# Kernel optimization log

Hardware: AMD Instinct MI355X
Metric: run time of the kernel (lower is better)

Reference implementation:

```python
import jax, jax.numpy as jnp
import numpy as np

D_MODEL = 512
D_FF = 2048
VOCAB = 32000
B, N = 2, 384
EPS = 1e-6


def positional_encoding(n, d):
    pos = np.arange(n)[:, None].astype(np.float64)
    i = np.arange(d)[None, :]
    ang = pos / np.power(10000.0, (2 * (i // 2)) / np.float32(d))
    ang[:, 0::2] = np.sin(ang[:, 0::2])
    ang[:, 1::2] = np.cos(ang[:, 1::2])
    return jnp.asarray(ang, dtype=jnp.float32)  # [n, d]


def layer_norm(x, gamma, beta):
    mu = jnp.mean(x, axis=-1, keepdims=True)
    var = jnp.mean(jnp.square(x - mu), axis=-1, keepdims=True)
    return (x - mu) / jnp.sqrt(var + EPS) * gamma + beta


def setup_inputs() -> dict:
    key = jax.random.key(0)
    ks = jax.random.split(key, 12)
    s = 0.02
    return {
        "tokens": jax.random.randint(ks[0], (B, N), 0, VOCAB, dtype=jnp.int32),
        "emb": jax.random.normal(ks[1], (VOCAB, D_MODEL), jnp.float32) * s,
        "Wq": jax.random.normal(ks[2], (D_MODEL, D_MODEL), jnp.float32) * s,
        "bq": jnp.zeros((D_MODEL,), jnp.float32),
        "Wk": jax.random.normal(ks[3], (D_MODEL, D_MODEL), jnp.float32) * s,
        "bk": jnp.zeros((D_MODEL,), jnp.float32),
        "Wv": jax.random.normal(ks[4], (D_MODEL, D_MODEL), jnp.float32) * s,
        "bv": jnp.zeros((D_MODEL,), jnp.float32),
        "attn_scale": jax.random.normal(ks[5], (D_MODEL,), jnp.float32) * 0.05,
        "Wo": jax.random.normal(ks[6], (D_MODEL, D_MODEL), jnp.float32) * s,
        "bo": jnp.zeros((D_MODEL,), jnp.float32),
        "g1": jnp.ones((D_MODEL,), jnp.float32),
        "beta1": jnp.zeros((D_MODEL,), jnp.float32),
        "W1": jax.random.normal(ks[7], (D_MODEL, D_FF), jnp.float32) * s,
        "bf1": jnp.zeros((D_FF,), jnp.float32),
        "W2": jax.random.normal(ks[8], (D_FF, D_MODEL), jnp.float32) * s,
        "bf2": jnp.zeros((D_MODEL,), jnp.float32),
        "g2": jnp.ones((D_MODEL,), jnp.float32),
        "beta2": jnp.zeros((D_MODEL,), jnp.float32),
    }


def reference(tokens, emb, Wq, bq, Wk, bk, Wv, bv, attn_scale, Wo, bo,
              g1, beta1, W1, bf1, W2, bf2, g2, beta2):
    # Embedding + scaled positional encoding
    x = emb[tokens] * jnp.sqrt(jnp.float32(D_MODEL))  # [B, N, D]
    x = x + positional_encoding(N, D_MODEL)[None, :, :]

    # Additive (Bahdanau) self-attention
    q = x @ Wq + bq
    k = x @ Wk + bk  # note: original swaps key/value Dense layers; math-equivalent
    v = x @ Wv + bv
    # scores[b,i,j] = sum_d scale[d] * tanh(q[b,i,d] + k[b,j,d])  -> [B,N,N]
    scores = jnp.einsum("d,bijd->bij", attn_scale,
                        jnp.tanh(q[:, :, None, :] + k[:, None, :, :]))
    weights = jax.nn.softmax(scores, axis=-1)
    attn = jnp.einsum("bij,bjd->bid", weights, v)
    attn = attn @ Wo + bo
    x = layer_norm(x + attn, g1, beta1)

    # Feedforward + residual + LayerNorm
    h = jax.nn.relu(x @ W1 + bf1)
    y = h @ W2 + bf2
    return layer_norm(x + y, g2, beta2)
```

## Files before the change

### kernel.cpp

```cpp
#include <hip/hip_runtime.h>
#include <hip/hip_bf16.h>
#include <math.h>

#define D_MODEL 512
#define D_FF    2048
#define NBATCH  2
#define NSEQ    384
#define NROWS   (NBATCH * NSEQ)
#define LN_EPS  1e-6f

typedef __attribute__((ext_vector_type(8))) short short8;
typedef __attribute__((ext_vector_type(4))) short short4v;
typedef __attribute__((ext_vector_type(4))) float f32x4;
typedef __hip_bfloat16 bf16;

static __device__ __forceinline__ short bfb(float x) {
    bf16 h = __float2bfloat16(x);
    return *reinterpret_cast<short*>(&h);
}

__global__ __launch_bounds__(256) void prep_kernel(
    const int* __restrict__ tokens, const float* __restrict__ emb,
    const float* __restrict__ Wq, const float* __restrict__ Wk,
    const float* __restrict__ Wv, const float* __restrict__ Wo,
    const float* __restrict__ W1, const float* __restrict__ W2,
    bf16* __restrict__ wqt, bf16* __restrict__ wkt, bf16* __restrict__ wvt,
    bf16* __restrict__ wot, bf16* __restrict__ w1t, bf16* __restrict__ w2t,
    float* __restrict__ x, bf16* __restrict__ xb)
{
    __shared__ float tile[32][33];
    int t = blockIdx.x;

    if (t < 3072) {
        const float* W; bf16* Wt; int K, N, bx, by;
        if (t < 1024) {
            int w = t >> 8, rem = t & 255;
            W  = (w == 0) ? Wq  : (w == 1) ? Wk  : (w == 2) ? Wv  : Wo;
            Wt = (w == 0) ? wqt : (w == 1) ? wkt : (w == 2) ? wvt : wot;
            K = 512; N = 512; bx = rem & 15; by = rem >> 4;
        } else if (t < 2048) {
            int rem = t - 1024;
            W = W1; Wt = w1t; K = 512; N = 2048; bx = rem & 63; by = rem >> 6;
        } else {
            int rem = t - 2048;
            W = W2; Wt = w2t; K = 2048; N = 512; bx = rem & 15; by = rem >> 4;
        }
        int tx = threadIdx.x & 31, ty = threadIdx.x >> 5;
        #pragma unroll
        for (int r = ty; r < 32; r += 8)
            tile[r][tx] = W[(size_t)(by * 32 + r) * N + bx * 32 + tx];
        __syncthreads();
        #pragma unroll
        for (int r = ty; r < 32; r += 8)
            Wt[(size_t)(bx * 32 + r) * K + by * 32 + tx] = __float2bfloat16(tile[tx][r]);
    } else {
        int row = t - 3072;
        int n   = row % NSEQ;
        int tok = tokens[row];
        const float sqrtD = 22.627416997969522f;
        const float ESC   = 0.02595256324130752f;
        for (int d = threadIdx.x; d < D_MODEL; d += 256) {
            float e   = emb[tok * D_MODEL + d] * sqrtD;
            float ang = (float)n * __builtin_amdgcn_exp2f(-(float)(d & ~1) * ESC);
            float pe  = (d & 1) ? __cosf(ang) : __sinf(ang);
            float val = e + pe;
            x [(size_t)row * D_MODEL + d] = val;
            xb[(size_t)row * D_MODEL + d] = __float2bfloat16(val);
        }
    }
}

__global__ __launch_bounds__(256) void qkv_mfma_kernel(
    const bf16* __restrict__ A,
    const bf16* __restrict__ wqt, const bf16* __restrict__ wkt, const bf16* __restrict__ wvt,
    const float* __restrict__ bq, const float* __restrict__ bk, const float* __restrict__ bv,
    float* __restrict__ aexp, float* __restrict__ bexp, bf16* __restrict__ vT)
{
    int z = blockIdx.z;
    const bf16*  Wt   = (z == 0) ? wqt : (z == 1) ? wkt : wvt;
    const float* bias = (z == 0) ? bq  : (z == 1) ? bk  : bv;

    int lane = threadIdx.x & 63, wid = threadIdx.x >> 6;
    int rowBase = blockIdx.y * 32 + (wid >> 1) * 16;
    int colBase = blockIdx.x * 64 + (wid & 1) * 32;

    const bf16* Ap  = A  + (size_t)(rowBase + (lane & 15)) * D_MODEL + ((lane >> 4) << 3);
    const bf16* Bp0 = Wt + (size_t)(colBase + (lane & 15)) * D_MODEL + ((lane >> 4) << 3);
    const bf16* Bp1 = Bp0 + (size_t)16 * D_MODEL;

    f32x4 acc0 = {0.f, 0.f, 0.f, 0.f};
    f32x4 acc1 = {0.f, 0.f, 0.f, 0.f};

    #pragma unroll 4
    for (int k0 = 0; k0 < D_MODEL; k0 += 32) {
        short8 a  = *reinterpret_cast<const short8*>(Ap  + k0);
        short8 b0 = *reinterpret_cast<const short8*>(Bp0 + k0);
        short8 b1 = *reinterpret_cast<const short8*>(Bp1 + k0);
        acc0 = __builtin_amdgcn_mfma_f32_16x16x32_bf16(a, b0, acc0, 0, 0, 0);
        acc1 = __builtin_amdgcn_mfma_f32_16x16x32_bf16(a, b1, acc1, 0, 0, 0);
    }

    int crow = rowBase + ((lane >> 4) << 2);
    int ccol = colBase + (lane & 15);

    if (z < 2) {
        float* C = (z == 0) ? aexp : bexp;
        #pragma unroll
        for (int r = 0; r < 4; ++r) {
            int row = crow + r;
            #pragma unroll
            for (int j = 0; j < 2; ++j) {
                int col = ccol + j * 16;
                float val = (j == 0 ? acc0[r] : acc1[r]) + bias[col];
                C[(size_t)row * D_MODEL + col] = __expf(2.0f * val);
            }
        }
    } else {
        int bb = crow / NSEQ;
        int jr = crow - bb * NSEQ;
        #pragma unroll
        for (int j = 0; j < 2; ++j) {
            int col = ccol + j * 16;
            short4v pk;
            #pragma unroll
            for (int r = 0; r < 4; ++r)
                pk[r] = bfb((j == 0 ? acc0[r] : acc1[r]) + bias[col]);
            size_t idx = ((size_t)bb * D_MODEL + col) * NSEQ + jr;
            *reinterpret_cast<short4v*>((short*)vT + idx) = pk;
        }
    }
}

__global__ __launch_bounds__(512) void score_kernel(
    const float* __restrict__ aexp, const float* __restrict__ bexp,
    const float* __restrict__ scale, bf16* __restrict__ E,
    float* __restrict__ Sp)
{
    int ig   = blockIdx.x;
    int qt   = blockIdx.y;
    int row0 = ig * 4;
    int b    = row0 / NSEQ;
    int tid  = threadIdx.x;
    int lane = tid & 63, wid = tid >> 6;

    __shared__ float sred[8][4];

    const float* ap = aexp + (size_t)row0 * D_MODEL + lane * 8;
    float a[4][8];
    #pragma unroll
    for (int r = 0; r < 4; ++r) {
        float4 A0 = *(const float4*)(ap + (size_t)r * D_MODEL);
        float4 A1 = *(const float4*)(ap + (size_t)r * D_MODEL + 4);
        a[r][0]=A0.x; a[r][1]=A0.y; a[r][2]=A0.z; a[r][3]=A0.w;
        a[r][4]=A1.x; a[r][5]=A1.y; a[r][6]=A1.z; a[r][7]=A1.w;
    }
    float4 S0 = *(const float4*)(scale + lane * 8);
    float4 S1 = *(const float4*)(scale + lane * 8 + 4);
    float sv[8] = {-2.0f*S0.x,-2.0f*S0.y,-2.0f*S0.z,-2.0f*S0.w,
                   -2.0f*S1.x,-2.0f*S1.y,-2.0f*S1.z,-2.0f*S1.w};

    const float* kb = bexp + (size_t)b * NSEQ * D_MODEL + lane * 8;
    int jb = qt * 96 + wid;

    float es[4] = {0.f, 0.f, 0.f, 0.f};

    for (int t6 = 0; t6 < 6; ++t6) {
        int j0 = jb + t6 * 16;
        int j1 = j0 + 8;
        const float4* kp0 = (const float4*)(kb + (size_t)j0 * D_MODEL);
        const float4* kp1 = (const float4*)(kb + (size_t)j1 * D_MODEL);
        float4 xa = kp0[0], xc = kp0[1];
        float4 ya = kp1[0], yc = kp1[1];
        float b0[8] = {xa.x,xa.y,xa.z,xa.w,xc.x,xc.y,xc.z,xc.w};
        float b1[8] = {ya.x,ya.y,ya.z,ya.w,yc.x,yc.y,yc.z,yc.w};

        float u[4][2] = {};
        #pragma unroll
        for (int up = 0; up < 4; ++up) {
            int d0 = up * 2, d1 = d0 + 1;
            #pragma unroll
            for (int js = 0; js < 2; ++js) {
                float xx = js ? b1[d0] : b0[d0];
                float yy = js ? b1[d1] : b0[d1];
                #pragma unroll
                for (int r = 0; r < 4; ++r) {
                    float p   = fmaf(a[r][d0], xx, 1.0f);
                    float q   = fmaf(a[r][d1], yy, 1.0f);
                    float num = fmaf(sv[d0], q, sv[d1] * p);
                    u[r][js]  = fmaf(num, __builtin_amdgcn_rcpf(p * q), u[r][js]);
                }
            }
        }

        #pragma unroll
        for (int off = 1; off < 64; off <<= 1) {
            #pragma unroll
            for (int r = 0; r < 4; ++r) {
                u[r][0] += __shfl_xor(u[r][0], off, 64);
                u[r][1] += __shfl_xor(u[r][1], off, 64);
            }
        }

        #pragma unroll
        for (int r = 0; r < 4; ++r) {
            float e0 = __expf(u[r][0]);
            float e1 = __expf(u[r][1]);
            if (lane == 0) {
                E[(size_t)(row0 + r) * NSEQ + j0] = __float2bfloat16(e0);
                E[(size_t)(row0 + r) * NSEQ + j1] = __float2bfloat16(e1);
            }
            es[r] += e0 + e1;
        }
    }

    if (lane == 0) {
        sred[wid][0] = es[0]; sred[wid][1] = es[1];
        sred[wid][2] = es[2]; sred[wid][3] = es[3];
    }
    __syncthreads();
    if (tid < 4) {
        float s = 0.0f;
        #pragma unroll
        for (int w = 0; w < 8; ++w) s += sred[w][tid];
        Sp[(size_t)(row0 + tid) * 4 + qt] = s;
    }
}

__global__ __launch_bounds__(256) void pv_mfma_kernel(
    const bf16* __restrict__ E, const bf16* __restrict__ vT,
    const float* __restrict__ Sp, bf16* __restrict__ attnb)
{
    int z = blockIdx.z;
    int lane = threadIdx.x & 63, wid = threadIdx.x >> 6;
    int rowBase = blockIdx.y * 32 + (wid >> 1) * 16;
    int colBase = blockIdx.x * 64 + (wid & 1) * 32;

    const bf16* Ap  = E  + ((size_t)z * NSEQ + rowBase + (lane & 15)) * NSEQ + ((lane >> 4) << 3);
    const bf16* Bp0 = vT + ((size_t)z * D_MODEL + colBase + (lane & 15)) * NSEQ + ((lane >> 4) << 3);
    const bf16* Bp1 = Bp0 + (size_t)16 * NSEQ;

    f32x4 acc0 = {0.f, 0.f, 0.f, 0.f};
    f32x4 acc1 = {0.f, 0.f, 0.f, 0.f};

    #pragma unroll 4
    for (int k0 = 0; k0 < NSEQ; k0 += 32) {
        short8 a  = *reinterpret_cast<const short8*>(Ap  + k0);
        short8 b0 = *reinterpret_cast<const short8*>(Bp0 + k0);
        short8 b1 = *reinterpret_cast<const short8*>(Bp1 + k0);
        acc0 = __builtin_amdgcn_mfma_f32_16x16x32_bf16(a, b0, acc0, 0, 0, 0);
        acc1 = __builtin_amdgcn_mfma_f32_16x16x32_bf16(a, b1, acc1, 0, 0, 0);
    }

    int crow = rowBase + ((lane >> 4) << 2);
    int ccol = colBase + (lane & 15);
    #pragma unroll
    for (int r = 0; r < 4; ++r) {
        int grow = z * NSEQ + crow + r;
        float4 sp4 = *(const float4*)(Sp + (size_t)grow * 4);
        float Sinv = 1.0f / (sp4.x + sp4.y + sp4.z + sp4.w);
        #pragma unroll
        for (int j = 0; j < 2; ++j)
            attnb[(size_t)grow * D_MODEL + ccol + j * 16] =
                __float2bfloat16((j == 0 ? acc0[r] : acc1[r]) * Sinv);
    }
}

__global__ __launch_bounds__(256) void mfma_gemm_kernel(
    const bf16* __restrict__ A, const bf16* __restrict__ Wt,
    const float* __restrict__ bias, const float* __restrict__ resid,
    float* __restrict__ Cf, bf16* __restrict__ Cb,
    int K, int N, int relu)
{
    int lane = threadIdx.x & 63, wid = threadIdx.x >> 6;
    int rowBase = blockIdx.y * 32 + (wid >> 1) * 16;
    int colBase = blockIdx.x * 64 + (wid & 1) * 32;

    const bf16* Ap  = A  + (size_t)(rowBase + (lane & 15)) * K + ((lane >> 4) << 3);
    const bf16* Bp0 = Wt + (size_t)(colBase + (lane & 15)) * K + ((lane >> 4) << 3);
    const bf16* Bp1 = Bp0 + (size_t)16 * K;

    f32x4 acc0 = {0.f, 0.f, 0.f, 0.f};
    f32x4 acc1 = {0.f, 0.f, 0.f, 0.f};

    #pragma unroll 4
    for (int k0 = 0; k0 < K; k0 += 32) {
        short8 a  = *reinterpret_cast<const short8*>(Ap  + k0);
        short8 b0 = *reinterpret_cast<const short8*>(Bp0 + k0);
        short8 b1 = *reinterpret_cast<const short8*>(Bp1 + k0);
        acc0 = __builtin_amdgcn_mfma_f32_16x16x32_bf16(a, b0, acc0, 0, 0, 0);
        acc1 = __builtin_amdgcn_mfma_f32_16x16x32_bf16(a, b1, acc1, 0, 0, 0);
    }

    int crow = rowBase + ((lane >> 4) << 2);
    int ccol = colBase + (lane & 15);
    #pragma unroll
    for (int r = 0; r < 4; ++r) {
        int row = crow + r;
        #pragma unroll
        for (int j = 0; j < 2; ++j) {
            int col = ccol + j * 16;
            float val = (j == 0 ? acc0[r] : acc1[r]) + bias[col];
            if (resid) val += resid[(size_t)row * N + col];
            if (relu)  val = fmaxf(val, 0.0f);
            if (Cf) Cf[(size_t)row * N + col] = val;
            if (Cb) Cb[(size_t)row * N + col] = __float2bfloat16(val);
        }
    }
}

__global__ __launch_bounds__(256) void ln_kernel(
    const float* __restrict__ in, const float* __restrict__ gamma,
    const float* __restrict__ beta, float* __restrict__ out,
    bf16* __restrict__ outb)
{
    int row = blockIdx.x;
    int tid = threadIdx.x;
    int lane = tid & 63, wid = tid >> 6;
    __shared__ float red[4];

    float v0 = in[(size_t)row * D_MODEL + tid];
    float v1 = in[(size_t)row * D_MODEL + tid + 256];

    float s = v0 + v1;
    #pragma unroll
    for (int off = 32; off; off >>= 1) s += __shfl_xor(s, off, 64);
    if (lane == 0) red[wid] = s;
    __syncthreads();
    if (tid == 0) red[0] = red[0] + red[1] + red[2] + red[3];
    __syncthreads();
    float mu = red[0] * (1.0f / D_MODEL);
    __syncthreads();

    float d0 = v0 - mu, d1 = v1 - mu;
    float s2 = d0 * d0 + d1 * d1;
    #pragma unroll
    for (int off = 32; off; off >>= 1) s2 += __shfl_xor(s2, off, 64);
    if (lane == 0) red[wid] = s2;
    __syncthreads();
    if (tid == 0) red[0] = red[0] + red[1] + red[2] + red[3];
    __syncthreads();
    float var = red[0] * (1.0f / D_MODEL);
    float inv = rsqrtf(var + LN_EPS);

    float o0 = d0 * inv * gamma[tid] + beta[tid];
    float o1 = d1 * inv * gamma[tid + 256] + beta[tid + 256];
    out[(size_t)row * D_MODEL + tid]       = o0;
    out[(size_t)row * D_MODEL + tid + 256] = o1;
    if (outb) {
        outb[(size_t)row * D_MODEL + tid]       = __float2bfloat16(o0);
        outb[(size_t)row * D_MODEL + tid + 256] = __float2bfloat16(o1);
    }
}

extern "C" void kernel_launch(void* const* d_in, const int* in_sizes, int n_in,
                              void* d_out, int out_size, void* d_ws, size_t ws_size,
                              hipStream_t stream)
{
    const int*   tokens = (const int*)  d_in[0];
    const float* emb    = (const float*)d_in[1];
    const float* Wq     = (const float*)d_in[2];
    const float* bq     = (const float*)d_in[3];
    const float* Wk     = (const float*)d_in[4];
    const float* bk     = (const float*)d_in[5];
    const float* Wv     = (const float*)d_in[6];
    const float* bv     = (const float*)d_in[7];
    const float* ascale = (const float*)d_in[8];
    const float* Wo     = (const float*)d_in[9];
    const float* bo     = (const float*)d_in[10];
    const float* g1     = (const float*)d_in[11];
    const float* beta1  = (const float*)d_in[12];
    const float* W1     = (const float*)d_in[13];
    const float* bf1    = (const float*)d_in[14];
    const float* W2     = (const float*)d_in[15];
    const float* bf2    = (const float*)d_in[16];
    const float* g2     = (const float*)d_in[17];
    const float* beta2  = (const float*)d_in[18];

    float* out = (float*)d_out;
    float* ws  = (float*)d_ws;

    const size_t SZ = (size_t)NROWS * D_MODEL;

    float* x0   = ws;
    float* aexp = ws + 1 * SZ;
    float* bexp = ws + 2 * SZ;
    float* t1 = aexp;
    float* x1 = bexp;
    float* y  = x0;

    bf16* x0b   = (bf16*)(ws + 3 * SZ);
    bf16* attnb = x0b + SZ;
    bf16* x1b   = attnb + SZ;
    bf16* hb    = x1b + SZ;
    bf16* Eb    = hb + (size_t)NROWS * D_FF;
    bf16* vTb   = Eb + (size_t)NBATCH * NSEQ * NSEQ;
    bf16* wqt   = vTb + (size_t)NBATCH * D_MODEL * NSEQ;
    bf16* wkt   = wqt + (size_t)D_MODEL * D_MODEL;
    bf16* wvt   = wkt + (size_t)D_MODEL * D_MODEL;
    bf16* wot   = wvt + (size_t)D_MODEL * D_MODEL;
    bf16* w1t   = wot + (size_t)D_MODEL * D_MODEL;
    bf16* w2t   = w1t + (size_t)D_MODEL * D_FF;
    float* Sp   = (float*)(w2t + (size_t)D_FF * D_MODEL);

    prep_kernel<<<3072 + NROWS, 256, 0, stream>>>(
        tokens, emb, Wq, Wk, Wv, Wo, W1, W2,
        wqt, wkt, wvt, wot, w1t, w2t, x0, x0b);

    qkv_mfma_kernel<<<dim3(D_MODEL / 64, NROWS / 32, 3), 256, 0, stream>>>(
        x0b, wqt, wkt, wvt, bq, bk, bv, aexp, bexp, vTb);

    score_kernel<<<dim3(NROWS / 4, 4), 512, 0, stream>>>(aexp, bexp, ascale, Eb, Sp);

    pv_mfma_kernel<<<dim3(D_MODEL / 64, NSEQ / 32, NBATCH), 256, 0, stream>>>(
        Eb, vTb, Sp, attnb);

    mfma_gemm_kernel<<<dim3(D_MODEL / 64, NROWS / 32), 256, 0, stream>>>(
        attnb, wot, bo, x0, t1, nullptr, D_MODEL, D_MODEL, 0);

    ln_kernel<<<NROWS, 256, 0, stream>>>(t1, g1, beta1, x1, x1b);

    mfma_gemm_kernel<<<dim3(D_FF / 64, NROWS / 32), 256, 0, stream>>>(
        x1b, w1t, bf1, nullptr, nullptr, hb, D_MODEL, D_FF, 1);

    mfma_gemm_kernel<<<dim3(D_MODEL / 64, NROWS / 32), 256, 0, stream>>>(
        hb, w2t, bf2, x1, y, nullptr, D_FF, D_MODEL, 0);

    ln_kernel<<<NROWS, 256, 0, stream>>>(y, g2, beta2, out, nullptr);
}
```

Before: 125.8 us.

## Fuse PV, Wo projection and first LayerNorm; split-K the FF down GEMM

Attention-weighted V, the Wo projection with bias and residual, and the first LayerNorm now run in one kernel. Each 512-thread block handles 16 rows and keeps the intermediate attention output and pre-norm activations in shared memory. This removes two launches and the global round trips for attnb and t1, at the cost of only 48 blocks, which may leave much of the GPU idle. The FF down-projection is split into two K halves to double the block count, and the partial sums are added inside the final LayerNorm kernel.

```diff
diff --git a/kernel.cpp b/kernel.cpp
--- a/kernel.cpp
+++ b/kernel.cpp
@@ -18,6 +18,8 @@
     bf16 h = __float2bfloat16(x);
     return *reinterpret_cast<short*>(&h);
 }
+
+#define MFMA16(a, b, c) __builtin_amdgcn_mfma_f32_16x16x32_bf16((a), (b), (c), 0, 0, 0)
 
 __global__ __launch_bounds__(256) void prep_kernel(
     const int* __restrict__ tokens, const float* __restrict__ emb,
@@ -96,8 +98,8 @@
         short8 a  = *reinterpret_cast<const short8*>(Ap  + k0);
         short8 b0 = *reinterpret_cast<const short8*>(Bp0 + k0);
         short8 b1 = *reinterpret_cast<const short8*>(Bp1 + k0);
-        acc0 = __builtin_amdgcn_mfma_f32_16x16x32_bf16(a, b0, acc0, 0, 0, 0);
-        acc1 = __builtin_amdgcn_mfma_f32_16x16x32_bf16(a, b1, acc1, 0, 0, 0);
+        acc0 = MFMA16(a, b0, acc0);
+        acc1 = MFMA16(a, b1, acc1);
     }
 
     int crow = rowBase + ((lane >> 4) << 2);
@@ -226,50 +228,117 @@
     }
 }
 
-__global__ __launch_bounds__(256) void pv_mfma_kernel(
+__global__ __launch_bounds__(512) void pv_wo_ln_kernel(
     const bf16* __restrict__ E, const bf16* __restrict__ vT,
-    const float* __restrict__ Sp, bf16* __restrict__ attnb)
-{
-    int z = blockIdx.z;
-    int lane = threadIdx.x & 63, wid = threadIdx.x >> 6;
-    int rowBase = blockIdx.y * 32 + (wid >> 1) * 16;
-    int colBase = blockIdx.x * 64 + (wid & 1) * 32;
-
-    const bf16* Ap  = E  + ((size_t)z * NSEQ + rowBase + (lane & 15)) * NSEQ + ((lane >> 4) << 3);
-    const bf16* Bp0 = vT + ((size_t)z * D_MODEL + colBase + (lane & 15)) * NSEQ + ((lane >> 4) << 3);
-    const bf16* Bp1 = Bp0 + (size_t)16 * NSEQ;
-
-    f32x4 acc0 = {0.f, 0.f, 0.f, 0.f};
-    f32x4 acc1 = {0.f, 0.f, 0.f, 0.f};
-
-    #pragma unroll 4
-    for (int k0 = 0; k0 < NSEQ; k0 += 32) {
-        short8 a  = *reinterpret_cast<const short8*>(Ap  + k0);
-        short8 b0 = *reinterpret_cast<const short8*>(Bp0 + k0);
-        short8 b1 = *reinterpret_cast<const short8*>(Bp1 + k0);
-        acc0 = __builtin_amdgcn_mfma_f32_16x16x32_bf16(a, b0, acc0, 0, 0, 0);
-        acc1 = __builtin_amdgcn_mfma_f32_16x16x32_bf16(a, b1, acc1, 0, 0, 0);
-    }
-
-    int crow = rowBase + ((lane >> 4) << 2);
-    int ccol = colBase + (lane & 15);
+    const float* __restrict__ Sp, const bf16* __restrict__ wot,
+    const float* __restrict__ bo, const float* __restrict__ x0,
+    const float* __restrict__ g1, const float* __restrict__ beta1,
+    float* __restrict__ x1, bf16* __restrict__ x1b)
+{
+    int row0 = blockIdx.x * 16;
+    int b    = row0 / NSEQ;
+    int tid  = threadIdx.x;
+    int lane = tid & 63, wid = tid >> 6;
+    int colBase = wid * 64;
+
+    __shared__ bf16  attnS[16][D_MODEL + 8];
+    __shared__ float t1f  [16][D_MODEL + 4];
+
+    int arow = lane & 15;
+    int koff = (lane >> 4) << 3;
+    int crow = (lane >> 4) << 2;
+    int ccol = lane & 15;
+
+    {
+        const bf16* Ap = E + ((size_t)(row0 + arow)) * NSEQ + koff;
+        const bf16* Bp = vT + ((size_t)b * D_MODEL + colBase + arow) * NSEQ + koff;
+        f32x4 p0 = {0,0,0,0}, p1 = {0,0,0,0}, p2 = {0,0,0,0}, p3 = {0,0,0,0};
+        #pragma unroll
+        for (int k0 = 0; k0 < NSEQ; k0 += 32) {
+            short8 a  = *(const short8*)(Ap + k0);
+            short8 v0 = *(const short8*)(Bp + k0);
+            short8 v1 = *(const short8*)(Bp + (size_t)16 * NSEQ + k0);
+            short8 v2 = *(const short8*)(Bp + (size_t)32 * NSEQ + k0);
+            short8 v3 = *(const short8*)(Bp + (size_t)48 * NSEQ + k0);
+            p0 = MFMA16(a, v0, p0);
+            p1 = MFMA16(a, v1, p1);
+            p2 = MFMA16(a, v2, p2);
+            p3 = MFMA16(a, v3, p3);
+        }
+        #pragma unroll
+        for (int r = 0; r < 4; ++r) {
+            int lrow = crow + r;
+            float4 sp4 = *(const float4*)(Sp + (size_t)(row0 + lrow) * 4);
+            float Sinv = 1.0f / (sp4.x + sp4.y + sp4.z + sp4.w);
+            attnS[lrow][colBase +  0 + ccol] = __float2bfloat16(p0[r] * Sinv);
+            attnS[lrow][colBase + 16 + ccol] = __float2bfloat16(p1[r] * Sinv);
+            attnS[lrow][colBase + 32 + ccol] = __float2bfloat16(p2[r] * Sinv);
+            attnS[lrow][colBase + 48 + ccol] = __float2bfloat16(p3[r] * Sinv);
+        }
+    }
+    __syncthreads();
+
+    {
+        const bf16* Wp = wot + ((size_t)(colBase + arow)) * D_MODEL + koff;
+        f32x4 w0 = {0,0,0,0}, w1 = {0,0,0,0}, w2 = {0,0,0,0}, w3 = {0,0,0,0};
+        #pragma unroll
+        for (int k0 = 0; k0 < D_MODEL; k0 += 32) {
+            short8 a  = *(const short8*)(&attnS[arow][k0 + koff]);
+            short8 q0 = *(const short8*)(Wp + k0);
+            short8 q1 = *(const short8*)(Wp + (size_t)16 * D_MODEL + k0);
+            short8 q2 = *(const short8*)(Wp + (size_t)32 * D_MODEL + k0);
+            short8 q3 = *(const short8*)(Wp + (size_t)48 * D_MODEL + k0);
+            w0 = MFMA16(a, q0, w0);
+            w1 = MFMA16(a, q1, w1);
+            w2 = MFMA16(a, q2, w2);
+            w3 = MFMA16(a, q3, w3);
+        }
+        #pragma unroll
+        for (int r = 0; r < 4; ++r) {
+            int lrow = crow + r;
+            size_t grow = (size_t)(row0 + lrow);
+            int c0 = colBase + ccol;
+            t1f[lrow][c0     ] = w0[r] + bo[c0     ] + x0[grow * D_MODEL + c0     ];
+            t1f[lrow][c0 + 16] = w1[r] + bo[c0 + 16] + x0[grow * D_MODEL + c0 + 16];
+            t1f[lrow][c0 + 32] = w2[r] + bo[c0 + 32] + x0[grow * D_MODEL + c0 + 32];
+            t1f[lrow][c0 + 48] = w3[r] + bo[c0 + 48] + x0[grow * D_MODEL + c0 + 48];
+        }
+    }
+    __syncthreads();
+
     #pragma unroll
-    for (int r = 0; r < 4; ++r) {
-        int grow = z * NSEQ + crow + r;
-        float4 sp4 = *(const float4*)(Sp + (size_t)grow * 4);
-        float Sinv = 1.0f / (sp4.x + sp4.y + sp4.z + sp4.w);
-        #pragma unroll
-        for (int j = 0; j < 2; ++j)
-            attnb[(size_t)grow * D_MODEL + ccol + j * 16] =
-                __float2bfloat16((j == 0 ? acc0[r] : acc1[r]) * Sinv);
+    for (int rr = 0; rr < 2; ++rr) {
+        int lrow = wid * 2 + rr;
+        size_t grow = (size_t)(row0 + lrow);
+        float v[8];
+        #pragma unroll
+        for (int u = 0; u < 8; ++u) v[u] = t1f[lrow][lane * 8 + u];
+        float s = 0.0f;
+        #pragma unroll
+        for (int u = 0; u < 8; ++u) s += v[u];
+        #pragma unroll
+        for (int off = 1; off < 64; off <<= 1) s += __shfl_xor(s, off, 64);
+        float mu = s * (1.0f / D_MODEL);
+        float s2 = 0.0f;
+        #pragma unroll
+        for (int u = 0; u < 8; ++u) { float d = v[u] - mu; s2 += d * d; }
+        #pragma unroll
+        for (int off = 1; off < 64; off <<= 1) s2 += __shfl_xor(s2, off, 64);
+        float inv = rsqrtf(s2 * (1.0f / D_MODEL) + LN_EPS);
+        #pragma unroll
+        for (int u = 0; u < 8; ++u) {
+            int c = lane * 8 + u;
+            float o = (v[u] - mu) * inv * g1[c] + beta1[c];
+            x1 [grow * D_MODEL + c] = o;
+            x1b[grow * D_MODEL + c] = __float2bfloat16(o);
+        }
     }
 }
 
 __global__ __launch_bounds__(256) void mfma_gemm_kernel(
     const bf16* __restrict__ A, const bf16* __restrict__ Wt,
-    const float* __restrict__ bias, const float* __restrict__ resid,
-    float* __restrict__ Cf, bf16* __restrict__ Cb,
-    int K, int N, int relu)
+    const float* __restrict__ bias,
+    bf16* __restrict__ Cb, int K, int N, int relu)
 {
     int lane = threadIdx.x & 63, wid = threadIdx.x >> 6;
     int rowBase = blockIdx.y * 32 + (wid >> 1) * 16;
@@ -287,8 +356,8 @@
         short8 a  = *reinterpret_cast<const short8*>(Ap  + k0);
         short8 b0 = *reinterpret_cast<const short8*>(Bp0 + k0);
         short8 b1 = *reinterpret_cast<const short8*>(Bp1 + k0);
-        acc0 = __builtin_amdgcn_mfma_f32_16x16x32_bf16(a, b0, acc0, 0, 0, 0);
-        acc1 = __builtin_amdgcn_mfma_f32_16x16x32_bf16(a, b1, acc1, 0, 0, 0);
+        acc0 = MFMA16(a, b0, acc0);
+        acc1 = MFMA16(a, b1, acc1);
     }
 
     int crow = rowBase + ((lane >> 4) << 2);
@@ -300,18 +369,62 @@
         for (int j = 0; j < 2; ++j) {
             int col = ccol + j * 16;
             float val = (j == 0 ? acc0[r] : acc1[r]) + bias[col];
-            if (resid) val += resid[(size_t)row * N + col];
-            if (relu)  val = fmaxf(val, 0.0f);
-            if (Cf) Cf[(size_t)row * N + col] = val;
-            if (Cb) Cb[(size_t)row * N + col] = __float2bfloat16(val);
+            if (relu) val = fmaxf(val, 0.0f);
+            Cb[(size_t)row * N + col] = __float2bfloat16(val);
+        }
+    }
+}
+
+__global__ __launch_bounds__(256) void ffdown_kernel(
+    const bf16* __restrict__ A, const bf16* __restrict__ Wt,
+    const float* __restrict__ bias, const float* __restrict__ resid,
+    float* __restrict__ y0, float* __restrict__ y1)
+{
+    int z = blockIdx.z;
+    int kbeg = z * (D_FF / 2);
+    int lane = threadIdx.x & 63, wid = threadIdx.x >> 6;
+    int rowBase = blockIdx.y * 32 + (wid >> 1) * 16;
+    int colBase = blockIdx.x * 64 + (wid & 1) * 32;
+
+    const bf16* Ap  = A  + (size_t)(rowBase + (lane & 15)) * D_FF + kbeg + ((lane >> 4) << 3);
+    const bf16* Bp0 = Wt + (size_t)(colBase + (lane & 15)) * D_FF + kbeg + ((lane >> 4) << 3);
+    const bf16* Bp1 = Bp0 + (size_t)16 * D_FF;
+
+    f32x4 acc0 = {0.f, 0.f, 0.f, 0.f};
+    f32x4 acc1 = {0.f, 0.f, 0.f, 0.f};
+
+    #pragma unroll 4
+    for (int k0 = 0; k0 < D_FF / 2; k0 += 32) {
+        short8 a  = *reinterpret_cast<const short8*>(Ap  + k0);
+        short8 b0 = *reinterpret_cast<const short8*>(Bp0 + k0);
+        short8 b1 = *reinterpret_cast<const short8*>(Bp1 + k0);
+        acc0 = MFMA16(a, b0, acc0);
+        acc1 = MFMA16(a, b1, acc1);
+    }
+
+    int crow = rowBase + ((lane >> 4) << 2);
+    int ccol = colBase + (lane & 15);
+    #pragma unroll
+    for (int r = 0; r < 4; ++r) {
+        int row = crow + r;
+        #pragma unroll
+        for (int j = 0; j < 2; ++j) {
+            int col = ccol + j * 16;
+            float val = (j == 0 ? acc0[r] : acc1[r]);
+            if (z == 0) {
+                val += bias[col] + resid[(size_t)row * D_MODEL + col];
+                y0[(size_t)row * D_MODEL + col] = val;
+            } else {
+                y1[(size_t)row * D_MODEL + col] = val;
+            }
         }
     }
 }
 
 __global__ __launch_bounds__(256) void ln_kernel(
-    const float* __restrict__ in, const float* __restrict__ gamma,
-    const float* __restrict__ beta, float* __restrict__ out,
-    bf16* __restrict__ outb)
+    const float* __restrict__ in, const float* __restrict__ in2,
+    const float* __restrict__ gamma, const float* __restrict__ beta,
+    float* __restrict__ out)
 {
     int row = blockIdx.x;
     int tid = threadIdx.x;
@@ -320,6 +433,10 @@
 
     float v0 = in[(size_t)row * D_MODEL + tid];
     float v1 = in[(size_t)row * D_MODEL + tid + 256];
+    if (in2) {
+        v0 += in2[(size_t)row * D_MODEL + tid];
+        v1 += in2[(size_t)row * D_MODEL + tid + 256];
+    }
 
     float s = v0 + v1;
     #pragma unroll
@@ -342,14 +459,8 @@
     float var = red[0] * (1.0f / D_MODEL);
     float inv = rsqrtf(var + LN_EPS);
 
-    float o0 = d0 * inv * gamma[tid] + beta[tid];
-    float o1 = d1 * inv * gamma[tid + 256] + beta[tid + 256];
-    out[(size_t)row * D_MODEL + tid]       = o0;
-    out[(size_t)row * D_MODEL + tid + 256] = o1;
-    if (outb) {
-        outb[(size_t)row * D_MODEL + tid]       = __float2bfloat16(o0);
-        outb[(size_t)row * D_MODEL + tid + 256] = __float2bfloat16(o1);
-    }
+    out[(size_t)row * D_MODEL + tid]       = d0 * inv * gamma[tid] + beta[tid];
+    out[(size_t)row * D_MODEL + tid + 256] = d1 * inv * gamma[tid + 256] + beta[tid + 256];
 }
 
 extern "C" void kernel_launch(void* const* d_in, const int* in_sizes, int n_in,
@@ -384,13 +495,12 @@
     float* x0   = ws;
     float* aexp = ws + 1 * SZ;
     float* bexp = ws + 2 * SZ;
-    float* t1 = aexp;
-    float* x1 = bexp;
-    float* y  = x0;
+    float* x1 = aexp;
+    float* y0 = x1;
+    float* y1 = bexp;
 
     bf16* x0b   = (bf16*)(ws + 3 * SZ);
-    bf16* attnb = x0b + SZ;
-    bf16* x1b   = attnb + SZ;
+    bf16* x1b   = x0b + SZ;
     bf16* hb    = x1b + SZ;
     bf16* Eb    = hb + (size_t)NROWS * D_FF;
     bf16* vTb   = Eb + (size_t)NBATCH * NSEQ * NSEQ;
@@ -411,19 +521,14 @@
 
     score_kernel<<<dim3(NROWS / 4, 4), 512, 0, stream>>>(aexp, bexp, ascale, Eb, Sp);
 
-    pv_mfma_kernel<<<dim3(D_MODEL / 64, NSEQ / 32, NBATCH), 256, 0, stream>>>(
-        Eb, vTb, Sp, attnb);
-
-    mfma_gemm_kernel<<<dim3(D_MODEL / 64, NROWS / 32), 256, 0, stream>>>(
-        attnb, wot, bo, x0, t1, nullptr, D_MODEL, D_MODEL, 0);
-
-    ln_kernel<<<NROWS, 256, 0, stream>>>(t1, g1, beta1, x1, x1b);
+    pv_wo_ln_kernel<<<NROWS / 16, 512, 0, stream>>>(
+        Eb, vTb, Sp, wot, bo, x0, g1, beta1, x1, x1b);
 
     mfma_gemm_kernel<<<dim3(D_FF / 64, NROWS / 32), 256, 0, stream>>>(
-        x1b, w1t, bf1, nullptr, nullptr, hb, D_MODEL, D_FF, 1);
-
-    mfma_gemm_kernel<<<dim3(D_MODEL / 64, NROWS / 32), 256, 0, stream>>>(
-        hb, w2t, bf2, x1, y, nullptr, D_FF, D_MODEL, 0);
-
-    ln_kernel<<<NROWS, 256, 0, stream>>>(y, g2, beta2, out, nullptr);
-}
+        x1b, w1t, bf1, hb, D_MODEL, D_FF, 1);
+
+    ffdown_kernel<<<dim3(D_MODEL / 64, NROWS / 32, 2), 256, 0, stream>>>(
+        hb, w2t, bf2, x1, y0, y1);
+
+    ln_kernel<<<NROWS, 256, 0, stream>>>(y0, y1, g2, beta2, out);
+}
```

After: 134.2 us. +6.7%, slower.

## Split-K the FF down GEMM and batch score shuffle reductions

Applied to the files above, without the earlier changes.

The FF down-projection GEMM becomes a two-way split-K kernel that doubles the block count. The two partial sums are added inside the final LayerNorm kernel, which gains an optional second input. Separately, the score kernel now runs three key tiles before doing their butterfly shuffle reductions together, which raises instruction-level parallelism but needs more registers. The split-K path also adds an extra fp32 partial buffer write and read, and its residual output aliases the residual input buffer.

```diff
diff --git a/kernel.cpp b/kernel.cpp
--- a/kernel.cpp
+++ b/kernel.cpp
@@ -18,6 +18,8 @@
     bf16 h = __float2bfloat16(x);
     return *reinterpret_cast<short*>(&h);
 }
+
+#define MFMA16(a, b, c) __builtin_amdgcn_mfma_f32_16x16x32_bf16((a), (b), (c), 0, 0, 0)
 
 __global__ __launch_bounds__(256) void prep_kernel(
     const int* __restrict__ tokens, const float* __restrict__ emb,
@@ -96,8 +98,8 @@
         short8 a  = *reinterpret_cast<const short8*>(Ap  + k0);
         short8 b0 = *reinterpret_cast<const short8*>(Bp0 + k0);
         short8 b1 = *reinterpret_cast<const short8*>(Bp1 + k0);
-        acc0 = __builtin_amdgcn_mfma_f32_16x16x32_bf16(a, b0, acc0, 0, 0, 0);
-        acc1 = __builtin_amdgcn_mfma_f32_16x16x32_bf16(a, b1, acc1, 0, 0, 0);
+        acc0 = MFMA16(a, b0, acc0);
+        acc1 = MFMA16(a, b1, acc1);
     }
 
     int crow = rowBase + ((lane >> 4) << 2);
@@ -164,52 +166,72 @@
 
     float es[4] = {0.f, 0.f, 0.f, 0.f};
 
-    for (int t6 = 0; t6 < 6; ++t6) {
-        int j0 = jb + t6 * 16;
-        int j1 = j0 + 8;
-        const float4* kp0 = (const float4*)(kb + (size_t)j0 * D_MODEL);
-        const float4* kp1 = (const float4*)(kb + (size_t)j1 * D_MODEL);
-        float4 xa = kp0[0], xc = kp0[1];
-        float4 ya = kp1[0], yc = kp1[1];
-        float b0[8] = {xa.x,xa.y,xa.z,xa.w,xc.x,xc.y,xc.z,xc.w};
-        float b1[8] = {ya.x,ya.y,ya.z,ya.w,yc.x,yc.y,yc.z,yc.w};
-
-        float u[4][2] = {};
-        #pragma unroll
-        for (int up = 0; up < 4; ++up) {
-            int d0 = up * 2, d1 = d0 + 1;
+    #pragma unroll
+    for (int half = 0; half < 2; ++half) {
+        float uacc[3][4][2];
+        #pragma unroll
+        for (int t3 = 0; t3 < 3; ++t3)
             #pragma unroll
-            for (int js = 0; js < 2; ++js) {
-                float xx = js ? b1[d0] : b0[d0];
-                float yy = js ? b1[d1] : b0[d1];
+            for (int r = 0; r < 4; ++r) {
+                uacc[t3][r][0] = 0.f; uacc[t3][r][1] = 0.f;
+            }
+
+        #pragma unroll
+        for (int t3 = 0; t3 < 3; ++t3) {
+            int t6 = half * 3 + t3;
+            int j0 = jb + t6 * 16;
+            int j1 = j0 + 8;
+            const float4* kp0 = (const float4*)(kb + (size_t)j0 * D_MODEL);
+            const float4* kp1 = (const float4*)(kb + (size_t)j1 * D_MODEL);
+            float4 xa = kp0[0], xc = kp0[1];
+            float4 ya = kp1[0], yc = kp1[1];
+            float b0[8] = {xa.x,xa.y,xa.z,xa.w,xc.x,xc.y,xc.z,xc.w};
+            float b1[8] = {ya.x,ya.y,ya.z,ya.w,yc.x,yc.y,yc.z,yc.w};
+
+            #pragma unroll
+            for (int up = 0; up < 4; ++up) {
+                int d0 = up * 2, d1 = d0 + 1;
+                #pragma unroll
+                for (int js = 0; js < 2; ++js) {
+                    float xx = js ? b1[d0] : b0[d0];
+                    float yy = js ? b1[d1] : b0[d1];
+                    #pragma unroll
+                    for (int r = 0; r < 4; ++r) {
+                        float p   = fmaf(a[r][d0], xx, 1.0f);
+                        float q   = fmaf(a[r][d1], yy, 1.0f);
+                        float num = fmaf(sv[d0], q, sv[d1] * p);
+                        uacc[t3][r][js] = fmaf(num, __builtin_amdgcn_rcpf(p * q),
+                                               uacc[t3][r][js]);
+                    }
+                }
+            }
+        }
+
+        #pragma unroll
+        for (int off = 1; off < 64; off <<= 1)
+            #pragma unroll
+            for (int t3 = 0; t3 < 3; ++t3)
                 #pragma unroll
                 for (int r = 0; r < 4; ++r) {
-                    float p   = fmaf(a[r][d0], xx, 1.0f);
-                    float q   = fmaf(a[r][d1], yy, 1.0f);
-                    float num = fmaf(sv[d0], q, sv[d1] * p);
-                    u[r][js]  = fmaf(num, __builtin_amdgcn_rcpf(p * q), u[r][js]);
+                    uacc[t3][r][0] += __shfl_xor(uacc[t3][r][0], off, 64);
+                    uacc[t3][r][1] += __shfl_xor(uacc[t3][r][1], off, 64);
                 }
-            }
-        }
-
-        #pragma unroll
-        for (int off = 1; off < 64; off <<= 1) {
+
+        #pragma unroll
+        for (int t3 = 0; t3 < 3; ++t3) {
+            int t6 = half * 3 + t3;
+            int j0 = jb + t6 * 16;
+            int j1 = j0 + 8;
             #pragma unroll
             for (int r = 0; r < 4; ++r) {
-                u[r][0] += __shfl_xor(u[r][0], off, 64);
-                u[r][1] += __shfl_xor(u[r][1], off, 64);
+                float e0 = __expf(uacc[t3][r][0]);
+                float e1 = __expf(uacc[t3][r][1]);
+                if (lane == 0) {
+                    E[(size_t)(row0 + r) * NSEQ + j0] = __float2bfloat16(e0);
+                    E[(size_t)(row0 + r) * NSEQ + j1] = __float2bfloat16(e1);
+                }
+                es[r] += e0 + e1;
             }
-        }
-
-        #pragma unroll
-        for (int r = 0; r < 4; ++r) {
-            float e0 = __expf(u[r][0]);
-            float e1 = __expf(u[r][1]);
-            if (lane == 0) {
-                E[(size_t)(row0 + r) * NSEQ + j0] = __float2bfloat16(e0);
-                E[(size_t)(row0 + r) * NSEQ + j1] = __float2bfloat16(e1);
-            }
-            es[r] += e0 + e1;
         }
     }
 
@@ -247,8 +269,8 @@
         short8 a  = *reinterpret_cast<const short8*>(Ap  + k0);
         short8 b0 = *reinterpret_cast<const short8*>(Bp0 + k0);
         short8 b1 = *reinterpret_cast<const short8*>(Bp1 + k0);
-        acc0 = __builtin_amdgcn_mfma_f32_16x16x32_bf16(a, b0, acc0, 0, 0, 0);
-        acc1 = __builtin_amdgcn_mfma_f32_16x16x32_bf16(a, b1, acc1, 0, 0, 0);
+        acc0 = MFMA16(a, b0, acc0);
+        acc1 = MFMA16(a, b1, acc1);
     }
 
     int crow = rowBase + ((lane >> 4) << 2);
@@ -287,8 +309,8 @@
         short8 a  = *reinterpret_cast<const short8*>(Ap  + k0);
         short8 b0 = *reinterpret_cast<const short8*>(Bp0 + k0);
         short8 b1 = *reinterpret_cast<const short8*>(Bp1 + k0);
-        acc0 = __builtin_amdgcn_mfma_f32_16x16x32_bf16(a, b0, acc0, 0, 0, 0);
-        acc1 = __builtin_amdgcn_mfma_f32_16x16x32_bf16(a, b1, acc1, 0, 0, 0);
+        acc0 = MFMA16(a, b0, acc0);
+        acc1 = MFMA16(a, b1, acc1);
     }
 
     int crow = rowBase + ((lane >> 4) << 2);
@@ -308,10 +330,56 @@
     }
 }
 
+__global__ __launch_bounds__(256) void ffdown_kernel(
+    const bf16* __restrict__ A, const bf16* __restrict__ Wt,
+    const float* __restrict__ bias, const float* __restrict__ resid,
+    float* __restrict__ y0, float* __restrict__ y1)
+{
+    int z = blockIdx.z;
+    int kbeg = z * (D_FF / 2);
+    int lane = threadIdx.x & 63, wid = threadIdx.x >> 6;
+    int rowBase = blockIdx.y * 32 + (wid >> 1) * 16;
+    int colBase = blockIdx.x * 64 + (wid & 1) * 32;
+
+    const bf16* Ap  = A  + (size_t)(rowBase + (lane & 15)) * D_FF + kbeg + ((lane >> 4) << 3);
+    const bf16* Bp0 = Wt + (size_t)(colBase + (lane & 15)) * D_FF + kbeg + ((lane >> 4) << 3);
+    const bf16* Bp1 = Bp0 + (size_t)16 * D_FF;
+
+    f32x4 acc0 = {0.f, 0.f, 0.f, 0.f};
+    f32x4 acc1 = {0.f, 0.f, 0.f, 0.f};
+
+    #pragma unroll 4
+    for (int k0 = 0; k0 < D_FF / 2; k0 += 32) {
+        short8 a  = *reinterpret_cast<const short8*>(Ap  + k0);
+        short8 b0 = *reinterpret_cast<const short8*>(Bp0 + k0);
+        short8 b1 = *reinterpret_cast<const short8*>(Bp1 + k0);
+        acc0 = MFMA16(a, b0, acc0);
+        acc1 = MFMA16(a, b1, acc1);
+    }
+
+    int crow = rowBase + ((lane >> 4) << 2);
+    int ccol = colBase + (lane & 15);
+    #pragma unroll
+    for (int r = 0; r < 4; ++r) {
+        int row = crow + r;
+        #pragma unroll
+        for (int j = 0; j < 2; ++j) {
+            int col = ccol + j * 16;
+            float val = (j == 0 ? acc0[r] : acc1[r]);
+            if (z == 0) {
+                val += bias[col] + resid[(size_t)row * D_MODEL + col];
+                y0[(size_t)row * D_MODEL + col] = val;
+            } else {
+                y1[(size_t)row * D_MODEL + col] = val;
+            }
+        }
+    }
+}
+
 __global__ __launch_bounds__(256) void ln_kernel(
-    const float* __restrict__ in, const float* __restrict__ gamma,
-    const float* __restrict__ beta, float* __restrict__ out,
-    bf16* __restrict__ outb)
+    const float* __restrict__ in, const float* __restrict__ in2,
+    const float* __restrict__ gamma, const float* __restrict__ beta,
+    float* __restrict__ out, bf16* __restrict__ outb)
 {
     int row = blockIdx.x;
     int tid = threadIdx.x;
@@ -320,6 +388,10 @@
 
     float v0 = in[(size_t)row * D_MODEL + tid];
     float v1 = in[(size_t)row * D_MODEL + tid + 256];
+    if (in2) {
+        v0 += in2[(size_t)row * D_MODEL + tid];
+        v1 += in2[(size_t)row * D_MODEL + tid + 256];
+    }
 
     float s = v0 + v1;
     #pragma unroll
@@ -386,7 +458,8 @@
     float* bexp = ws + 2 * SZ;
     float* t1 = aexp;
     float* x1 = bexp;
-    float* y  = x0;
+    float* y0 = x1;
+    float* y1 = x0;
 
     bf16* x0b   = (bf16*)(ws + 3 * SZ);
     bf16* attnb = x0b + SZ;
@@ -417,13 +490,13 @@
     mfma_gemm_kernel<<<dim3(D_MODEL / 64, NROWS / 32), 256, 0, stream>>>(
         attnb, wot, bo, x0, t1, nullptr, D_MODEL, D_MODEL, 0);
 
-    ln_kernel<<<NROWS, 256, 0, stream>>>(t1, g1, beta1, x1, x1b);
+    ln_kernel<<<NROWS, 256, 0, stream>>>(t1, nullptr, g1, beta1, x1, x1b);
 
     mfma_gemm_kernel<<<dim3(D_FF / 64, NROWS / 32), 256, 0, stream>>>(
         x1b, w1t, bf1, nullptr, nullptr, hb, D_MODEL, D_FF, 1);
 
-    mfma_gemm_kernel<<<dim3(D_MODEL / 64, NROWS / 32), 256, 0, stream>>>(
-        hb, w2t, bf2, x1, y, nullptr, D_FF, D_MODEL, 0);
-
-    ln_kernel<<<NROWS, 256, 0, stream>>>(y, g2, beta2, out, nullptr);
-}
+    ffdown_kernel<<<dim3(D_MODEL / 64, NROWS / 32, 2), 256, 0, stream>>>(
+        hb, w2t, bf2, x1, y0, y1);
+
+    ln_kernel<<<NROWS, 256, 0, stream>>>(y0, y1, g2, beta2, out, nullptr);
+}
```

Result: no change. 123.8 us (-1.6%).
